# Optimization experiments

Hardware: AMD Instinct MI355X
Metric: run time of the kernel (lower is better)

## Reference

```python
import math
import jax, jax.numpy as jnp
import numpy as np

H, D, HID, BLOCK = 32, 64, 2048, 256   # heads, head_dim, hidden(=h*d), chunk size
N = 8192                                # prefill sequence length
NUM_LAYERS, LAYER_IDX = 80, 0
EPS = 1e-5


def _build_slopes(n):
    def p2(m):
        start = 2 ** (-2 ** (-(math.log2(m) - 3)))
        return [start * start ** i for i in range(m)]
    if math.log2(n).is_integer():
        s = p2(n)
    else:
        cp = 2 ** math.floor(math.log2(n))
        s = p2(cp) + _build_slopes(2 * cp).tolist()[0::2][: n - cp]
    return np.array(s, dtype=np.float32)

SLOPE = jnp.asarray(_build_slopes(H) * (1.0 - LAYER_IDX / (NUM_LAYERS - 1) + 1e-5))  # [H]


def setup_inputs() -> dict:
    key = jax.random.key(0)
    ks = jax.random.split(key, 5)
    return {
        "hidden_states": jax.random.normal(ks[0], (N, HID), jnp.float32),
        "kv_cache": jnp.zeros((H, D, D), jnp.float32),
        "W_qkv": jax.random.normal(ks[1], (3 * HID, HID), jnp.float32) * 0.02,
        "W_gate": jax.random.normal(ks[2], (HID, HID), jnp.float32) * 0.02,
        "W_out": jax.random.normal(ks[3], (HID, HID), jnp.float32) * 0.02,
        "norm_weight": jnp.ones((HID,), jnp.float32),
    }


def lightning_attention(q, k, v, slope, kv0):
    # q,k,v: [h,n,d]; kv0: [h,d,d]; chunked linear attention with per-head decay
    h, n, d = q.shape
    nb = n // BLOCK
    arr = jnp.arange(BLOCK, dtype=jnp.float32) + 1.0          # 1..BLOCK
    s = slope[:, None, None]                                   # [h,1,1]
    q_decay = jnp.exp(-s * arr[None, :, None])                 # [h,B,1]
    k_decay = jnp.exp(-s * (BLOCK - arr)[None, :, None])       # [h,B,1]
    idx = arr[:, None] - arr[None, :]                          # [B,B]
    diag_decay = jnp.where(idx[None] >= 0, jnp.exp(-s * idx[None]), 0.0)  # [h,B,B]
    block_decay = jnp.exp(-slope * BLOCK)[:, None, None]       # [h,1,1]

    def to_blocks(x):
        return x.reshape(h, nb, BLOCK, d).transpose(1, 0, 2, 3)  # [nb,h,B,d]

    qb, kb, vb = to_blocks(q), to_blocks(k), to_blocks(v)

    def step(kv, blk):
        qi, ki, vi = blk                                        # [h,B,d]
        inter = jnp.einsum('hmd,hde->hme', qi * q_decay, kv)    # carry-state term
        qk = jnp.einsum('hmd,hnd->hmn', qi, ki) * diag_decay    # intra-block causal decayed scores
        intra = jnp.einsum('hmn,hne->hme', qk, vi)
        kv_new = block_decay * kv + jnp.einsum('hmd,hme->hde', ki * k_decay, vi)
        return kv_new, inter + intra

    kv_final, out = jax.lax.scan(step, kv0, (qb, kb, vb))
    out = out.transpose(1, 0, 2, 3).reshape(h, n, d)
    return out, kv_final


def reference(hidden_states, kv_cache, W_qkv, W_gate, W_out, norm_weight):
    # qkv projection + SiLU in fp32 (as in vLLM MiniMaxText01)
    qkv = jax.nn.silu((hidden_states @ W_qkv.T).astype(jnp.float32))  # [n, 3*HID]
    qkv = qkv.reshape(N, H, 3 * D)
    q, k, v = jnp.split(qkv, 3, axis=-1)                              # each [n,h,d]
    q, k, v = (t.transpose(1, 0, 2) for t in (q, k, v))               # [h,n,d]
    attn, _kv = lightning_attention(q, k, v, SLOPE, kv_cache)
    hidden = attn.transpose(1, 0, 2).reshape(N, H * D)                # 'h n d -> n (h d)'
    # RMSNorm (tp_world=1)
    var = jnp.mean(hidden * hidden, axis=-1, keepdims=True)
    hidden = hidden * jax.lax.rsqrt(var + EPS) * norm_weight
    gate = jax.nn.sigmoid(hidden_states @ W_gate.T)
    return (gate * hidden) @ W_out.T
```

## Files before the change

kernel.cpp:

```cpp
#include <hip/hip_runtime.h>

#define NTOK   8192
#define HIDDEN 2048
#define NHEAD  32
#define HDIM   64
#define BLK    256
#define NBLK   32
#define QKVW   6144

typedef unsigned short ushort_t;
typedef __attribute__((ext_vector_type(8))) short bf16x8;
typedef __attribute__((ext_vector_type(4))) float floatx4;
typedef __attribute__((ext_vector_type(4))) unsigned short ushortx4;

#define MFMA16(a, b, c) __builtin_amdgcn_mfma_f32_16x16x32_bf16(a, b, c, 0, 0, 0)

__device__ __forceinline__ float head_slope(int h) {
    return exp2f(-0.25f * (float)(h + 1)) * 1.00001f;
}

__device__ __forceinline__ ushort_t f2bf(float x) {
    unsigned int u = __float_as_uint(x);
    unsigned int r = (u + 0x7FFFu + ((u >> 16) & 1u)) >> 16;
    return (ushort_t)r;
}
__device__ __forceinline__ float bf2f(ushort_t x) {
    return __uint_as_float(((unsigned int)x) << 16);
}
__device__ __forceinline__ void store1(float* p, float v) { *p = v; }
__device__ __forceinline__ void store1(ushort_t* p, float v) { *p = f2bf(v); }

#define GLOAD_LDS16(g, l)                                              \
    __builtin_amdgcn_global_load_lds(                                  \
        (const __attribute__((address_space(1))) void*)(g),            \
        (__attribute__((address_space(3))) void*)(l), 16, 0, 0)

__global__ __launch_bounds__(256) void cvt_bf16(
    const float* __restrict__ in, ushort_t* __restrict__ out, int n8) {
    int i = blockIdx.x * 256 + threadIdx.x;
    if (i >= n8) return;
    long base = (long)i * 8;
    float4 a = *(const float4*)(in + base);
    float4 b = *(const float4*)(in + base + 4);
    ushort4 u0 = {f2bf(a.x), f2bf(a.y), f2bf(a.z), f2bf(a.w)};
    ushort4 u1 = {f2bf(b.x), f2bf(b.y), f2bf(b.z), f2bf(b.w)};
    *(ushort4*)(out + base) = u0;
    *(ushort4*)(out + base + 4) = u1;
}

template <int EPI, typename OutT>
__global__ __launch_bounds__(512, 2) void gemm256_bt(
    const ushort_t* __restrict__ A, const ushort_t* __restrict__ B,
    OutT* __restrict__ C, const float* __restrict__ Mul,
    int M, int Ncol, int K) {
    __shared__ __align__(128) ushort_t As[2][256 * 64];
    __shared__ __align__(128) ushort_t Bs[2][256 * 64];

    const int t = threadIdx.x;
    const int wave = t >> 6, lane = t & 63;
    const int wm = wave >> 2, wn = wave & 3;
    const int fm = lane & 15, quad = lane >> 4;

    const int nbn = Ncol >> 8;
    const int flat = blockIdx.y * gridDim.x + blockIdx.x;
    const int nwg = gridDim.x * gridDim.y;
    const int nid = (flat & 7) * (nwg >> 3) + (flat >> 3);
    const int bm = nid / nbn;
    const int bn = nid - bm * nbn;

    const int srow = t >> 3;
    const int schunk = ((t & 7) ^ (srow & 7)) << 3;
    const ushort_t* Ags = A + ((long)bm * 256 + srow) * K + schunk;
    const ushort_t* Bgs = B + ((long)bn * 256 + srow) * K + schunk;
    const int sdst = wave * 512;

#define STAGE_AQ(kt_, buf_, q_)                                          \
    GLOAD_LDS16(Ags + (long)(q_) * 64 * K + (long)(kt_) * 64,            \
                &As[buf_][(q_) * 4096 + sdst])
#define STAGE_BQ(kt_, buf_, q_)                                          \
    GLOAD_LDS16(Bgs + (long)(q_) * 64 * K + (long)(kt_) * 64,            \
                &Bs[buf_][(q_) * 4096 + sdst])

    const int aoff = (wm * 128 + fm) * 64;
    const int boff = (wn * 64 + fm) * 64;
    const int cx0 = ((quad ^ (fm & 7)) << 3);
    const int cx1 = (((4 + quad) ^ (fm & 7)) << 3);

    floatx4 acc[8][4];
#pragma unroll
    for (int i = 0; i < 8; i++)
#pragma unroll
        for (int j = 0; j < 4; j++) acc[i][j] = (floatx4){0.f, 0.f, 0.f, 0.f};

    const int NKT = K >> 6;
#pragma unroll
    for (int q = 0; q < 4; q++) STAGE_AQ(0, 0, q);
#pragma unroll
    for (int q = 0; q < 4; q++) STAGE_BQ(0, 0, q);
#pragma unroll
    for (int q = 0; q < 4; q++) STAGE_AQ(1, 1, q);
#pragma unroll
    for (int q = 0; q < 4; q++) STAGE_BQ(1, 1, q);
    asm volatile("s_waitcnt vmcnt(8)" ::: "memory");
    __builtin_amdgcn_s_barrier();

    for (int kt = 0; kt < NKT; ++kt) {
        const int cur = kt & 1;
        const ushort_t* Ab = &As[cur][0];
        const ushort_t* Bb = &Bs[cur][0];
        const bool st = (kt + 2 < NKT);

        bf16x8 a0[4][2], a1[4][2], bl[2][2], bh[2][2];

#pragma unroll
        for (int mt = 0; mt < 4; ++mt) {
            a0[mt][0] = *(const bf16x8*)&Ab[aoff + mt * 1024 + cx0];
            a0[mt][1] = *(const bf16x8*)&Ab[aoff + mt * 1024 + cx1];
        }
#pragma unroll
        for (int nt = 0; nt < 2; ++nt) {
            bl[nt][0] = *(const bf16x8*)&Bb[boff + nt * 1024 + cx0];
            bl[nt][1] = *(const bf16x8*)&Bb[boff + nt * 1024 + cx1];
        }
        asm volatile("s_waitcnt lgkmcnt(8)" ::: "memory");
        __builtin_amdgcn_s_barrier();
        asm volatile("s_waitcnt lgkmcnt(0)" ::: "memory");
        __builtin_amdgcn_sched_barrier(0);
        __builtin_amdgcn_s_setprio(1);
#pragma unroll
        for (int mt = 0; mt < 4; ++mt)
#pragma unroll
            for (int nt = 0; nt < 2; ++nt) {
                acc[mt][nt] = MFMA16(a0[mt][0], bl[nt][0], acc[mt][nt]);
                acc[mt][nt] = MFMA16(a0[mt][1], bl[nt][1], acc[mt][nt]);
            }
        __builtin_amdgcn_s_setprio(0);
        __builtin_amdgcn_s_barrier();

#pragma unroll
        for (int nt = 0; nt < 2; ++nt) {
            bh[nt][0] = *(const bf16x8*)&Bb[boff + 2048 + nt * 1024 + cx0];
            bh[nt][1] = *(const bf16x8*)&Bb[boff + 2048 + nt * 1024 + cx1];
        }
        if (st) { STAGE_AQ(kt + 2, cur, 0); STAGE_AQ(kt + 2, cur, 2); }
        __builtin_amdgcn_s_barrier();
        asm volatile("s_waitcnt lgkmcnt(0)" ::: "memory");
        __builtin_amdgcn_sched_barrier(0);
        __builtin_amdgcn_s_setprio(1);
#pragma unroll
        for (int mt = 0; mt < 4; ++mt)
#pragma unroll
            for (int nt = 0; nt < 2; ++nt) {
                acc[mt][2 + nt] = MFMA16(a0[mt][0], bh[nt][0], acc[mt][2 + nt]);
                acc[mt][2 + nt] = MFMA16(a0[mt][1], bh[nt][1], acc[mt][2 + nt]);
            }
        __builtin_amdgcn_s_setprio(0);
        __builtin_amdgcn_s_barrier();

#pragma unroll
        for (int mt = 0; mt < 4; ++mt) {
            a1[mt][0] = *(const bf16x8*)&Ab[aoff + 4096 + mt * 1024 + cx0];
            a1[mt][1] = *(const bf16x8*)&Ab[aoff + 4096 + mt * 1024 + cx1];
        }
        if (st) {
            STAGE_BQ(kt + 2, cur, 0); STAGE_BQ(kt + 2, cur, 1);
            STAGE_BQ(kt + 2, cur, 2); STAGE_BQ(kt + 2, cur, 3);
        }
        __builtin_amdgcn_s_barrier();
        asm volatile("s_waitcnt lgkmcnt(0)" ::: "memory");
        __builtin_amdgcn_sched_barrier(0);
        __builtin_amdgcn_s_setprio(1);
#pragma unroll
        for (int mt = 0; mt < 4; ++mt)
#pragma unroll
            for (int nt = 0; nt < 2; ++nt) {
                acc[4 + mt][2 + nt] = MFMA16(a1[mt][0], bh[nt][0], acc[4 + mt][2 + nt]);
                acc[4 + mt][2 + nt] = MFMA16(a1[mt][1], bh[nt][1], acc[4 + mt][2 + nt]);
            }
        __builtin_amdgcn_s_setprio(0);
        __builtin_amdgcn_s_barrier();

        if (st) { STAGE_AQ(kt + 2, cur, 1); STAGE_AQ(kt + 2, cur, 3); }
        __builtin_amdgcn_s_barrier();
        __builtin_amdgcn_sched_barrier(0);
        __builtin_amdgcn_s_setprio(1);
#pragma unroll
        for (int mt = 0; mt < 4; ++mt)
#pragma unroll
            for (int nt = 0; nt < 2; ++nt) {
                acc[4 + mt][nt] = MFMA16(a1[mt][0], bl[nt][0], acc[4 + mt][nt]);
                acc[4 + mt][nt] = MFMA16(a1[mt][1], bl[nt][1], acc[4 + mt][nt]);
            }
        __builtin_amdgcn_s_setprio(0);

        if (kt + 2 < NKT) {
            asm volatile("s_waitcnt vmcnt(8)" ::: "memory");
        } else if (kt + 1 < NKT) {
            asm volatile("s_waitcnt vmcnt(0)" ::: "memory");
        }
        __builtin_amdgcn_s_barrier();
    }
#undef STAGE_AQ
#undef STAGE_BQ

#pragma unroll
    for (int mt = 0; mt < 8; ++mt)
#pragma unroll
        for (int nt = 0; nt < 4; ++nt) {
            long col = (long)bn * 256 + wn * 64 + nt * 16 + fm;
#pragma unroll
            for (int r = 0; r < 4; ++r) {
                long row = (long)bm * 256 + wm * 128 + mt * 16 + quad * 4 + r;
                long idx = row * Ncol + col;
                float x = acc[mt][nt][r];
                float o;
                if (EPI == 0)      o = x / (1.f + expf(-x));
                else if (EPI == 1) o = x;
                else               o = Mul[idx] / (1.f + expf(-x));
                store1(C + idx, o);
            }
        }
}

__global__ __launch_bounds__(256) void attn_contrib_mfma(
    const ushort_t* __restrict__ qkv, float* __restrict__ contrib) {
    const int b = blockIdx.x, h = blockIdx.y;
    const float s = head_slope(h);
    __shared__ ushort_t kdT[64][72];
    __shared__ ushort_t vT[64][72];
    const int t = threadIdx.x, wave = t >> 6, lane = t & 63;
    const int fm = lane & 15, quad = lane >> 4;
    const ushort_t* base = qkv + (long)(b * BLK) * QKVW + h * (3 * HDIM);

    floatx4 acc[4];
#pragma unroll
    for (int e = 0; e < 4; e++) acc[e] = (floatx4){0.f, 0.f, 0.f, 0.f};

    const int sn = t & 63;
    const int sc0 = t >> 6;

    for (int tt = 0; tt < 4; tt++) {
        __syncthreads();
        int tok = tt * 64 + sn;
        float kd = expf(-s * (float)(BLK - 1 - tok));
#pragma unroll
        for (int cc = 0; cc < 2; cc++) {
            int c = sc0 + cc * 4;
            bf16x8 k8 = *(const bf16x8*)(base + (long)tok * QKVW + HDIM + c * 8);
            bf16x8 v8 = *(const bf16x8*)(base + (long)tok * QKVW + 2 * HDIM + c * 8);
#pragma unroll
            for (int j = 0; j < 8; j++) {
                kdT[c * 8 + j][sn] = f2bf(bf2f((ushort_t)k8[j]) * kd);
                vT[c * 8 + j][sn]  = (ushort_t)v8[j];
            }
        }
        __syncthreads();
#pragma unroll
        for (int kh = 0; kh < 2; kh++) {
            bf16x8 a = *(const bf16x8*)&kdT[wave * 16 + fm][kh * 32 + quad * 8];
#pragma unroll
            for (int e = 0; e < 4; e++) {
                bf16x8 bb = *(const bf16x8*)&vT[e * 16 + fm][kh * 32 + quad * 8];
                acc[e] = MFMA16(a, bb, acc[e]);
            }
        }
    }
    float* outp = contrib + ((long)(h * NBLK + b)) * 4096;
#pragma unroll
    for (int e = 0; e < 4; e++)
#pragma unroll
        for (int r = 0; r < 4; r++) {
            int d = wave * 16 + quad * 4 + r;
            outp[d * 64 + e * 16 + fm] = acc[e][r];
        }
}

__global__ __launch_bounds__(256) void attn_scan(
    const float* __restrict__ kv0, const float* __restrict__ contrib,
    float* __restrict__ states) {
    const int h = blockIdx.x, seg = blockIdx.y, t = threadIdx.x;
    const float s  = head_slope(h);
    const float bd = expf(-s * (float)BLK);
    const int off = seg * 1024 + t * 4;
    float4 st = *(const float4*)(kv0 + (long)h * 4096 + off);
    for (int b = 0; b < NBLK; b++) {
        const long base = ((long)(h * NBLK + b)) * 4096 + off;
        float4 c = *(const float4*)(contrib + base);
        *(float4*)(states + base) = st;
        st.x = bd * st.x + c.x;
        st.y = bd * st.y + c.y;
        st.z = bd * st.z + c.z;
        st.w = bd * st.w + c.w;
    }
}

__global__ __launch_bounds__(256) void attn_core_mfma(
    const ushort_t* __restrict__ qkv, const float* __restrict__ states,
    float* __restrict__ hidden) {
    const int b = blockIdx.x, h = blockIdx.y;
    const float s = head_slope(h);
    __shared__ ushort_t Sw[4][64][72];
    __shared__ ushort_t kS[64 * 64];
    __shared__ ushort_t vT[64][72];
    __shared__ float dtab[257];
    __shared__ float etab[64];
    const int t = threadIdx.x, wave = t >> 6, lane = t & 63;
    const int fm = lane & 15, quad = lane >> 4;
    const ushort_t* base = qkv + (long)(b * BLK) * QKVW + h * (3 * HDIM);

    dtab[t] = expf(-s * (float)t);
    if (t == 0) dtab[256] = expf(-s * 256.f);
    if (t < 64) etab[t] = expf(s * (float)t);

    {
        const float* sp = states + ((long)(h * NBLK + b)) * 4096;
#pragma unroll
        for (int i = 0; i < 4; i++) {
            int idx = t + 256 * i;
            int d = idx >> 4, e4 = (idx & 15) * 4;
            float4 st4 = *(const float4*)(sp + d * 64 + e4);
            Sw[0][e4 + 0][d] = f2bf(st4.x);
            Sw[0][e4 + 1][d] = f2bf(st4.y);
            Sw[0][e4 + 2][d] = f2bf(st4.z);
            Sw[0][e4 + 3][d] = f2bf(st4.w);
        }
    }

    bf16x8 aq[4][2];
#pragma unroll
    for (int mt = 0; mt < 4; mt++)
#pragma unroll
        for (int kh = 0; kh < 2; kh++)
            aq[mt][kh] = *(const bf16x8*)(base +
                (long)(wave * 64 + mt * 16 + fm) * QKVW + kh * 32 + quad * 8);

    __syncthreads();

    floatx4 acc[4][4];
#pragma unroll
    for (int i = 0; i < 4; i++)
#pragma unroll
        for (int j = 0; j < 4; j++) acc[i][j] = (floatx4){0.f, 0.f, 0.f, 0.f};
#pragma unroll
    for (int kh = 0; kh < 2; kh++)
#pragma unroll
        for (int et = 0; et < 4; et++) {
            bf16x8 bst = *(const bf16x8*)&Sw[0][et * 16 + fm][kh * 32 + quad * 8];
#pragma unroll
            for (int mt = 0; mt < 4; mt++)
                acc[mt][et] = MFMA16(aq[mt][kh], bst, acc[mt][et]);
        }
#pragma unroll
    for (int mt = 0; mt < 4; mt++)
#pragma unroll
        for (int r = 0; r < 4; r++) {
            float qd = dtab[wave * 64 + mt * 16 + quad * 4 + r + 1];
#pragma unroll
            for (int et = 0; et < 4; et++) acc[mt][et][r] *= qd;
        }

    const int sn = t & 63, sc0 = t >> 6;
    for (int nt = 0; nt < 4; nt++) {
        __syncthreads();
#pragma unroll
        for (int i = 0; i < 2; i++) {
            int row = i * 32 + wave * 8 + (lane >> 3);
            const ushort_t* g = base + (long)(nt * 64 + row) * QKVW + HDIM +
                                (((lane & 7) ^ (lane >> 3)) * 8);
            GLOAD_LDS16(g, &kS[(i * 32 + wave * 8) * 64]);
        }
#pragma unroll
        for (int cc = 0; cc < 2; cc++) {
            int c = sc0 + cc * 4;
            bf16x8 v8 = *(const bf16x8*)(base + (long)(nt * 64 + sn) * QKVW +
                                         2 * HDIM + c * 8);
#pragma unroll
            for (int j = 0; j < 8; j++) vT[c * 8 + j][sn] = (ushort_t)v8[j];
        }
        __syncthreads();

        if (nt <= wave) {
            floatx4 sacc[4][4];
#pragma unroll
            for (int i = 0; i < 4; i++)
#pragma unroll
                for (int j = 0; j < 4; j++) sacc[i][j] = (floatx4){0.f, 0.f, 0.f, 0.f};
#pragma unroll
            for (int kh = 0; kh < 2; kh++) {
                bf16x8 ak[4];
#pragma unroll
                for (int snt = 0; snt < 4; snt++) {
                    int n = snt * 16 + fm;
                    int pos = (kh * 4 + quad) ^ (n & 7);
                    ak[snt] = *(const bf16x8*)&kS[n * 64 + pos * 8];
                }
#pragma unroll
                for (int snt = 0; snt < 4; snt++)
#pragma unroll
                    for (int smt = 0; smt < 4; smt++)
                        sacc[snt][smt] = MFMA16(ak[snt], aq[smt][kh], sacc[snt][smt]);
            }
#pragma unroll
            for (int snt = 0; snt < 4; snt++)
#pragma unroll
                for (int smt = 0; smt < 4; smt++) {
                    int mloc = smt * 16 + fm;
                    float rf = dtab[wave * 64 + mloc - nt * 64];
                    ushortx4 o;
#pragma unroll
                    for (int r = 0; r < 4; r++) {
                        int nloc = snt * 16 + quad * 4 + r;
                        float v = sacc[snt][smt][r] * rf * etab[nloc];
                        if (nt == wave && mloc < nloc) v = 0.f;
                        o[r] = f2bf(v);
                    }
                    *(ushortx4*)&Sw[wave][mloc][snt * 16 + quad * 4] = o;
                }
#pragma unroll
            for (int kh = 0; kh < 2; kh++) {
                bf16x8 as[4];
#pragma unroll
                for (int mt = 0; mt < 4; mt++)
                    as[mt] = *(const bf16x8*)&Sw[wave][mt * 16 + fm][kh * 32 + quad * 8];
#pragma unroll
                for (int et = 0; et < 4; et++) {
                    bf16x8 bv = *(const bf16x8*)&vT[et * 16 + fm][kh * 32 + quad * 8];
#pragma unroll
                    for (int mt = 0; mt < 4; mt++)
                        acc[mt][et] = MFMA16(as[mt], bv, acc[mt][et]);
                }
            }
        }
    }

#pragma unroll
    for (int mt = 0; mt < 4; mt++)
#pragma unroll
        for (int r = 0; r < 4; r++) {
            long tok = (long)b * BLK + wave * 64 + mt * 16 + quad * 4 + r;
            float* hp = hidden + tok * HIDDEN + h * HDIM;
#pragma unroll
            for (int et = 0; et < 4; et++)
                hp[et * 16 + fm] = acc[mt][et][r];
        }
}

__global__ __launch_bounds__(256) void rmsnorm_rows(
    float* __restrict__ hidden, const float* __restrict__ w) {
    const int row = blockIdx.x, t = threadIdx.x;
    float* hp = hidden + (long)row * HIDDEN;
    float4 a = *(const float4*)(hp + (t << 2));
    float4 b = *(const float4*)(hp + 1024 + (t << 2));
    float ss = a.x * a.x + a.y * a.y + a.z * a.z + a.w * a.w +
               b.x * b.x + b.y * b.y + b.z * b.z + b.w * b.w;
#pragma unroll
    for (int off = 32; off > 0; off >>= 1) ss += __shfl_down(ss, off);
    __shared__ float red[4];
    if ((t & 63) == 0) red[t >> 6] = ss;
    __syncthreads();
    float tot = red[0] + red[1] + red[2] + red[3];
    float scale = rsqrtf(tot * (1.f / HIDDEN) + 1e-5f);
    float4 wa = *(const float4*)(w + (t << 2));
    float4 wb = *(const float4*)(w + 1024 + (t << 2));
    a.x *= scale * wa.x; a.y *= scale * wa.y; a.z *= scale * wa.z; a.w *= scale * wa.w;
    b.x *= scale * wb.x; b.y *= scale * wb.y; b.z *= scale * wb.z; b.w *= scale * wb.w;
    *(float4*)(hp + (t << 2)) = a;
    *(float4*)(hp + 1024 + (t << 2)) = b;
}

extern "C" void kernel_launch(void* const* d_in, const int* in_sizes, int n_in,
                              void* d_out, int out_size, void* d_ws, size_t ws_size,
                              hipStream_t stream) {
    (void)in_sizes; (void)n_in; (void)out_size; (void)ws_size;
    const float* hs   = (const float*)d_in[0];
    const float* kv0  = (const float*)d_in[1];
    const float* Wqkv = (const float*)d_in[2];
    const float* Wg   = (const float*)d_in[3];
    const float* Wo   = (const float*)d_in[4];
    const float* nw   = (const float*)d_in[5];
    float* out = (float*)d_out;

    ushort_t* hs_h   = (ushort_t*)d_ws;
    ushort_t* wqkv_h = hs_h + (size_t)NTOK * HIDDEN;
    ushort_t* wg_h   = wqkv_h + (size_t)QKVW * HIDDEN;
    ushort_t* wo_h   = wg_h + (size_t)HIDDEN * HIDDEN;
    ushort_t* qkv_h  = wo_h + (size_t)HIDDEN * HIDDEN;
    float*    cs     = (float*)(qkv_h + (size_t)NTOK * QKVW);
    ushort_t* gated  = qkv_h;

    cvt_bf16<<<(NTOK * HIDDEN / 8 + 255) / 256, 256, 0, stream>>>(
        hs, hs_h, NTOK * HIDDEN / 8);
    cvt_bf16<<<(QKVW * HIDDEN / 8 + 255) / 256, 256, 0, stream>>>(
        Wqkv, wqkv_h, QKVW * HIDDEN / 8);
    cvt_bf16<<<(HIDDEN * HIDDEN / 8 + 255) / 256, 256, 0, stream>>>(
        Wg, wg_h, HIDDEN * HIDDEN / 8);
    cvt_bf16<<<(HIDDEN * HIDDEN / 8 + 255) / 256, 256, 0, stream>>>(
        Wo, wo_h, HIDDEN * HIDDEN / 8);

    gemm256_bt<0, ushort_t><<<dim3(QKVW / 256, NTOK / 256), 512, 0, stream>>>(
        hs_h, wqkv_h, qkv_h, nullptr, NTOK, QKVW, HIDDEN);
    attn_contrib_mfma<<<dim3(NBLK, NHEAD), 256, 0, stream>>>(qkv_h, cs);
    attn_scan<<<dim3(NHEAD, 4), 256, 0, stream>>>(kv0, cs, cs);
    attn_core_mfma<<<dim3(NBLK, NHEAD), 256, 0, stream>>>(qkv_h, cs, out);
    rmsnorm_rows<<<NTOK, 256, 0, stream>>>(out, nw);
    gemm256_bt<2, ushort_t><<<dim3(HIDDEN / 256, NTOK / 256), 512, 0, stream>>>(
        hs_h, wg_h, gated, out, NTOK, HIDDEN, HIDDEN);
    gemm256_bt<1, float><<<dim3(HIDDEN / 256, NTOK / 256), 512, 0, stream>>>(
        gated, wo_h, out, nullptr, NTOK, HIDDEN, HIDDEN);
}
```

Before: 653.2 us.

## Fuse bf16 conversions into one launch and group GEMM tile order for L2 reuse

The four separate fp32-to-bf16 conversion launches become a single kernel. It writes into the contiguous workspace, which is laid out in the same order, so three launches and their tail gaps go away. The GEMM workgroup-to-tile mapping is also changed from a plain row-major order to groups of 8 M-tiles sharing each N column. The aim is better L2 reuse of A and B tiles across the XCD-interleaved dispatch. The grouped mapping assumes the M tile count is a multiple of 8, which holds for these sizes.

```diff
diff --git a/kernel.cpp b/kernel.cpp
--- a/kernel.cpp
+++ b/kernel.cpp
@@ -35,17 +35,30 @@
         (const __attribute__((address_space(1))) void*)(g),            \
         (__attribute__((address_space(3))) void*)(l), 16, 0, 0)
 
-__global__ __launch_bounds__(256) void cvt_bf16(
-    const float* __restrict__ in, ushort_t* __restrict__ out, int n8) {
+#define CVT_N0 (NTOK * HIDDEN / 8)
+#define CVT_N1 (QKVW * HIDDEN / 8)
+#define CVT_N2 (HIDDEN * HIDDEN / 8)
+#define CVT_NTOT (CVT_N0 + CVT_N1 + 2 * CVT_N2)
+
+__global__ __launch_bounds__(256) void cvt_bf16_all(
+    const float* __restrict__ s0, const float* __restrict__ s1,
+    const float* __restrict__ s2, const float* __restrict__ s3,
+    ushort_t* __restrict__ dst) {
     int i = blockIdx.x * 256 + threadIdx.x;
-    if (i >= n8) return;
-    long base = (long)i * 8;
-    float4 a = *(const float4*)(in + base);
-    float4 b = *(const float4*)(in + base + 4);
+    if (i >= CVT_NTOT) return;
+    const float* src;
+    long si;
+    if (i < CVT_N0)                    { src = s0; si = i; }
+    else if (i < CVT_N0 + CVT_N1)      { src = s1; si = i - CVT_N0; }
+    else if (i < CVT_N0 + CVT_N1 + CVT_N2) { src = s2; si = i - CVT_N0 - CVT_N1; }
+    else                               { src = s3; si = i - CVT_N0 - CVT_N1 - CVT_N2; }
+    float4 a = *(const float4*)(src + si * 8);
+    float4 b = *(const float4*)(src + si * 8 + 4);
     ushort4 u0 = {f2bf(a.x), f2bf(a.y), f2bf(a.z), f2bf(a.w)};
     ushort4 u1 = {f2bf(b.x), f2bf(b.y), f2bf(b.z), f2bf(b.w)};
-    *(ushort4*)(out + base) = u0;
-    *(ushort4*)(out + base + 4) = u1;
+    long base = (long)i * 8;
+    *(ushort4*)(dst + base) = u0;
+    *(ushort4*)(dst + base + 4) = u1;
 }
 
 template <int EPI, typename OutT>
@@ -62,11 +75,14 @@
     const int fm = lane & 15, quad = lane >> 4;
 
     const int nbn = Ncol >> 8;
+    const int nbm = M >> 8;
     const int flat = blockIdx.y * gridDim.x + blockIdx.x;
-    const int nwg = gridDim.x * gridDim.y;
-    const int nid = (flat & 7) * (nwg >> 3) + (flat >> 3);
-    const int bm = nid / nbn;
-    const int bn = nid - bm * nbn;
+    const int nwg = nbn * nbm;
+    const int r = (flat & 7) * (nwg >> 3) + (flat >> 3);
+    const int g = r / (8 * nbn);
+    const int rg = r - g * 8 * nbn;
+    const int bn = rg >> 3;
+    const int bm = g * 8 + (rg & 7);
 
     const int srow = t >> 3;
     const int schunk = ((t & 7) ^ (srow & 7)) << 3;
@@ -209,10 +225,10 @@
         for (int nt = 0; nt < 4; ++nt) {
             long col = (long)bn * 256 + wn * 64 + nt * 16 + fm;
 #pragma unroll
-            for (int r = 0; r < 4; ++r) {
-                long row = (long)bm * 256 + wm * 128 + mt * 16 + quad * 4 + r;
+            for (int r2 = 0; r2 < 4; ++r2) {
+                long row = (long)bm * 256 + wm * 128 + mt * 16 + quad * 4 + r2;
                 long idx = row * Ncol + col;
-                float x = acc[mt][nt][r];
+                float x = acc[mt][nt][r2];
                 float o;
                 if (EPI == 0)      o = x / (1.f + expf(-x));
                 else if (EPI == 1) o = x;
@@ -488,14 +504,8 @@
     float*    cs     = (float*)(qkv_h + (size_t)NTOK * QKVW);
     ushort_t* gated  = qkv_h;
 
-    cvt_bf16<<<(NTOK * HIDDEN / 8 + 255) / 256, 256, 0, stream>>>(
-        hs, hs_h, NTOK * HIDDEN / 8);
-    cvt_bf16<<<(QKVW * HIDDEN / 8 + 255) / 256, 256, 0, stream>>>(
-        Wqkv, wqkv_h, QKVW * HIDDEN / 8);
-    cvt_bf16<<<(HIDDEN * HIDDEN / 8 + 255) / 256, 256, 0, stream>>>(
-        Wg, wg_h, HIDDEN * HIDDEN / 8);
-    cvt_bf16<<<(HIDDEN * HIDDEN / 8 + 255) / 256, 256, 0, stream>>>(
-        Wo, wo_h, HIDDEN * HIDDEN / 8);
+    cvt_bf16_all<<<(CVT_NTOT + 255) / 256, 256, 0, stream>>>(
+        hs, Wqkv, Wg, Wo, hs_h);
 
     gemm256_bt<0, ushort_t><<<dim3(QKVW / 256, NTOK / 256), 512, 0, stream>>>(
         hs_h, wqkv_h, qkv_h, nullptr, NTOK, QKVW, HIDDEN);
```

New measurement: 625.5 us. -4.2%, faster.
